# Performance work log

Measured on AMD Instinct MI355X. Metric: run time of the kernel, lower is better.

The kernel has to match this reference:

```python
import jax, jax.numpy as jnp
import numpy as np

LORA_SCALING = 2.0

def setup_inputs() -> dict:
    key = jax.random.key(0)
    ks = jax.random.split(key, 10)
    B, T, C, H, R, E = 4, 2048, 2048, 8192, 64, 4
    f32 = jnp.float32
    def w(k, shape, fan_in):
        return jax.random.normal(k, shape, f32) / np.float32(np.sqrt(fan_in))
    return {
        "x": jax.random.normal(ks[0], (B, T, C), f32),
        "x_prev": jax.random.normal(ks[1], (B, C), f32),
        "x_k": jax.random.uniform(ks[2], (1, 1, C), f32),
        "Router_ref": w(ks[3], (E - 1, C), C),
        "K_ref": w(ks[4], (C, H), C),          # right-multiplied: h @ K_ref
        "V_ref": w(ks[5], (H, C), H),          # right-multiplied: k @ V_ref
        "Ka": w(ks[6], (E, R, C), C),          # torch Linear layout [out,in]
        "Kb": w(ks[7], (E, H, R), R),
        "Va": w(ks[8], (E, R, H), H),
        "Vb": w(ks[9], (E, C, R), R),
        "MoETopk": 2,
        "MoECount": 4,
    }

def _moe_forward(x, x_prev, x_k, Router_ref, K_ref, V_ref, Ka, Kb, Va, Vb, MoETopk, MoECount):
    B, T, C = x.shape
    # token shift: mix each token with the previous one (x_prev seeds t=0)
    xx = jnp.concatenate([x_prev[:, None, :], x[:, :-1, :]], axis=1) - x
    h = (x + xx * x_k).reshape(-1, C)  # [N, C], N = B*T tokens
    N = h.shape[0]

    # router: expert 0 has implicit score 0, experts 1..E-1 come from Router_ref
    scores = h @ Router_ref.T                                   # [N, E-1]
    scores_all = jnp.concatenate([jnp.zeros((N, 1), h.dtype), scores], axis=-1)  # [N, E]
    if MoETopk < MoECount:
        topv, topi = jax.lax.top_k(scores_all, MoETopk)         # [N, K]
        gate = jax.nn.softmax(topv, axis=-1)
        gating_full = jnp.zeros_like(scores_all).at[
            jnp.arange(N)[:, None], topi].set(gate)             # [N, E], 0 for unselected
    else:
        gating_full = jax.nn.softmax(scores_all, axis=-1)

    # dense combine: gating weight is exactly 0 for unselected experts, so this
    # matches the original sparse dispatch + index_add math bit-for-bit in value.
    out = jnp.zeros_like(h)
    for e in range(MoECount):  # small fixed expert count
        k_e = jax.nn.relu(h @ K_ref + LORA_SCALING * (h @ Ka[e].T) @ Kb[e].T) ** 2  # [N, H]
        v_e = k_e @ V_ref + LORA_SCALING * (k_e @ Va[e].T) @ Vb[e].T                # [N, C]
        out = out + gating_full[:, e:e + 1] * v_e
    return out.reshape(B, T, C), x[:, -1, :]

def reference(x, x_prev, x_k, Router_ref, K_ref, V_ref, Ka, Kb, Va, Vb, MoETopk, MoECount):
    return _moe_forward(x, x_prev, x_k, Router_ref, K_ref, V_ref, Ka, Kb, Va, Vb,
                        int(MoETopk), int(MoECount))
```

## Files before the change

### kernel.cpp

```cpp
#include <hip/hip_runtime.h>


#define DEV_INLINE __device__ __forceinline__

typedef __attribute__((ext_vector_type(8))) short bf16x8;
typedef __attribute__((ext_vector_type(4))) float f32x4;

DEV_INLINE unsigned short f2bf(float f) {
  union { float f; unsigned int u; } v; v.f = f;
  unsigned int u = v.u;
  unsigned int r = (u + 0x7FFFu + ((u >> 16) & 1u)) >> 16;
  return (unsigned short)r;
}
DEV_INLINE float bf2f(unsigned short s) {
  union { unsigned int u; float f; } v; v.u = ((unsigned int)s) << 16;
  return v.f;
}


__global__ __launch_bounds__(256) void prep_kernel(
    const float* __restrict__ x, const float* __restrict__ x_prev,
    const float* __restrict__ x_k, unsigned short* __restrict__ h, int n0) {
  const int idx = blockIdx.x * 256 + threadIdx.x;
  const int c4 = idx & 511;
  const int gn = n0 + (idx >> 9);
  const int t  = gn & 2047;
  const int b  = gn >> 11;
  const float4 cur = ((const float4*)x)[(size_t)gn * 512 + c4];
  const float4 prv = (t == 0) ? ((const float4*)x_prev)[(b << 9) + c4]
                              : ((const float4*)x)[(size_t)gn * 512 - 512 + c4];
  const float4 k = ((const float4*)x_k)[c4];
  float hx = cur.x + (prv.x - cur.x) * k.x;
  float hy = cur.y + (prv.y - cur.y) * k.y;
  float hz = cur.z + (prv.z - cur.z) * k.z;
  float hw = cur.w + (prv.w - cur.w) * k.w;
  uint2 o;
  o.x = (unsigned int)f2bf(hx) | ((unsigned int)f2bf(hy) << 16);
  o.y = (unsigned int)f2bf(hz) | ((unsigned int)f2bf(hw) << 16);
  ((uint2*)h)[idx] = o;
}

__global__ __launch_bounds__(256) void xlast_kernel(
    const float* __restrict__ x, float* __restrict__ x_last) {
  const int i = blockIdx.x * 256 + threadIdx.x;
  const int b = i >> 9, c4 = i & 511;
  ((float4*)x_last)[i] =
      ((const float4*)x)[((size_t)b * 2048 + 2047) * 512 + c4];
}

__global__ __launch_bounds__(256) void transpose_cast(
    const float* __restrict__ in, unsigned short* __restrict__ outp,
    int rows, int cols) {
  __shared__ float tile[32][33];
  const int bx = blockIdx.x * 32, by = blockIdx.y * 32;
  const int tx = threadIdx.x, ty = threadIdx.y;
#pragma unroll
  for (int k = 0; k < 4; ++k)
    tile[ty + k * 8][tx] = in[(size_t)(by + ty + k * 8) * cols + bx + tx];
  __syncthreads();
#pragma unroll
  for (int k = 0; k < 4; ++k)
    outp[(size_t)(bx + ty + k * 8) * rows + by + tx] = f2bf(tile[tx][ty + k * 8]);
}

__global__ __launch_bounds__(256) void cast_bf16(
    const float* __restrict__ in, unsigned short* __restrict__ outp, int n4) {
  const int i = blockIdx.x * 256 + threadIdx.x;
  if (i >= n4) return;
  const float4 v = ((const float4*)in)[i];
  uint2 o;
  o.x = (unsigned int)f2bf(v.x) | ((unsigned int)f2bf(v.y) << 16);
  o.y = (unsigned int)f2bf(v.z) | ((unsigned int)f2bf(v.w) << 16);
  ((uint2*)outp)[i] = o;
}

__global__ void zero_page(unsigned int* zp) {
  if (threadIdx.x < 64) zp[threadIdx.x] = 0;
}

__global__ __launch_bounds__(256) void router_kernel(
    const float* __restrict__ x, const float* __restrict__ x_prev,
    const float* __restrict__ x_k, const float* __restrict__ Rt,
    int* __restrict__ tbl, int* __restrict__ etok,
    float* __restrict__ gate_tok, int MC, int n0) {
  const int lane = threadIdx.x & 63, wid = threadIdx.x >> 6;
  const int nl = blockIdx.x * 4 + wid;
  const int gn = n0 + nl;
  const int t = gn & 2047, b = gn >> 11;
  const float* cur = x + (size_t)gn * 2048;
  const float* prv = (t == 0) ? x_prev + (size_t)b * 2048 : cur - 2048;
  float hv[32];
#pragma unroll
  for (int j = 0; j < 32; ++j) {
    const int i = j * 64 + lane;
    const float xc = cur[i];
    hv[j] = xc + (prv[i] - xc) * x_k[i];
  }
  float s[4];
  s[0] = 0.f;
  for (int e = 1; e < 4; ++e) {
    const float* rrow = Rt + (size_t)(e - 1) * 2048;
    float a = 0.f;
#pragma unroll
    for (int j = 0; j < 32; ++j) a += hv[j] * rrow[j * 64 + lane];
#pragma unroll
    for (int d = 32; d >= 1; d >>= 1) a += __shfl_xor(a, d, 64);
    s[e] = a;
  }
  if (lane == 0) {
    int i1 = 0; float v1 = s[0];
    for (int e = 1; e < 4; ++e) if (s[e] > v1) { v1 = s[e]; i1 = e; }
    int i2 = -1; float v2 = -1e30f;
    for (int e = 0; e < 4; ++e) if (e != i1 && s[e] > v2) { v2 = s[e]; i2 = e; }
    const float ex = expf(v2 - v1);
    const float g1 = 1.f / (1.f + ex), g2 = ex / (1.f + ex);
    etok[nl] = i1;          etok[MC + nl] = i2;
    gate_tok[nl] = g1;      gate_tok[MC + nl] = g2;
    atomicAdd(&tbl[i1], 1); atomicAdd(&tbl[4 + i2], 1);
  }
}

__global__ void zero_hist(int* tbl) {
  if (threadIdx.x < 8) tbl[threadIdx.x] = 0;
}

__global__ __launch_bounds__(128) void seg_build(int* __restrict__ tbl, int MB) {
  const int tid = threadIdx.x;
  __shared__ int sbase[2][5];
  if (tid == 0) {
    for (int k = 0; k < 2; ++k) {
      int b = 0; sbase[k][0] = 0;
      for (int e = 0; e < 4; ++e) {
        b += ((tbl[k * 4 + e] + 127) >> 7) << 7;
        sbase[k][e + 1] = b;
      }
      for (int e = 0; e < 5; ++e) tbl[16 + k * 5 + e] = sbase[k][e];
    }
    for (int i = 0; i < 8; ++i) tbl[8 + i] = 0;
  }
  __syncthreads();
  int* bt = tbl + 32;
  for (int i = tid; i < 2 * MB; i += 128) {
    const int k = i / MB, row = (i % MB) * 128;
    int e = -1;
    for (int q = 0; q < 4; ++q)
      if (row >= sbase[k][q] && row < sbase[k][q + 1]) e = q;
    bt[i] = e;
  }
  int* tok = tbl + 32 + 2 * MB;
  for (int i = tid; i < 2 * MB * 128; i += 128) tok[i] = -1;
}

__global__ __launch_bounds__(256) void scatter_build(
    int* __restrict__ tbl, const int* __restrict__ etok, int MC, int MB) {
  const int t = blockIdx.x * 256 + threadIdx.x;
  if (t >= MC) return;
  int* tok = tbl + 32 + 2 * MB;
#pragma unroll
  for (int k = 0; k < 2; ++k) {
    const int e = etok[k * MC + t];
    const int r = atomicAdd(&tbl[8 + k * 4 + e], 1);
    tok[k * MB * 128 + tbl[16 + k * 5 + e] + r] = t;
  }
}

__global__ __launch_bounds__(512, 1) void gemm256(
    const unsigned short* __restrict__ A, int lda,
    const unsigned short* __restrict__ Bt, int ldb,
    unsigned short* __restrict__ C, int ldc, int K, int nbx) {
  __shared__ char smem[2][2][256 * 64 * 2];
  const int nwg = gridDim.x, wg = blockIdx.x;
  const int q = nwg >> 3, r = nwg & 7;
  const int xcd = wg & 7, loc = wg >> 3;
  const int swz = (xcd < r ? xcd * (q + 1) : r * (q + 1) + (xcd - r) * q) + loc;
  const int bx = swz % nbx, by = swz / nbx;
  const int m0 = by * 256, n0 = bx * 256;
  const int tid = threadIdx.x, lane = tid & 63;
  const int wid = tid >> 6, wr = wid >> 2, wc = wid & 3;

  int arow[4], scol[4];
#pragma unroll
  for (int i = 0; i < 4; ++i) {
    const int qq = i * 512 + tid;
    const int row = qq >> 3, w = qq & 7;
    arow[i] = row;
    scol[i] = (w ^ (row & 7)) * 8;
  }

  f32x4 acc[8][4] = {};

  auto stage = [&](int buf, int kt) {
#pragma unroll
    for (int i = 0; i < 4; ++i) {
      const unsigned short* src =
          A + (size_t)(m0 + arow[i]) * lda + kt + scol[i];
      __builtin_amdgcn_global_load_lds(
          (const __attribute__((address_space(1))) void*)src,
          (__attribute__((address_space(3))) void*)(
              &smem[buf][0][(i * 512 + tid) * 16]), 16, 0, 0);
    }
#pragma unroll
    for (int i = 0; i < 4; ++i) {
      const unsigned short* src =
          Bt + (size_t)(n0 + arow[i]) * ldb + kt + scol[i];
      __builtin_amdgcn_global_load_lds(
          (const __attribute__((address_space(1))) void*)src,
          (__attribute__((address_space(3))) void*)(
              &smem[buf][1][(i * 512 + tid) * 16]), 16, 0, 0);
    }
  };

  stage(0, 0);
  asm volatile("s_waitcnt vmcnt(0)" ::: "memory");
  __syncthreads();

  const int NT = K >> 6;
  for (int t = 0; t < NT; ++t) {
    const int cur = t & 1;
    if (t + 1 < NT) stage(cur ^ 1, (t + 1) << 6);
    const char* As = smem[cur][0];
    const char* Bs = smem[cur][1];
#pragma unroll
    for (int ks = 0; ks < 2; ++ks) {
#pragma unroll
      for (int mh = 0; mh < 2; ++mh) {
        bf16x8 af[4];
#pragma unroll
        for (int m = 0; m < 4; ++m) {
          const int row = wr * 128 + mh * 64 + m * 16 + (lane & 15);
          const int kb = (ks * 64 + ((lane >> 4) * 16)) ^ ((row & 7) << 4);
          af[m] = *(const bf16x8*)(As + row * 128 + kb);
        }
#pragma unroll
        for (int nh = 0; nh < 2; ++nh) {
          bf16x8 bf[2];
#pragma unroll
          for (int n = 0; n < 2; ++n) {
            const int row = wc * 64 + nh * 32 + n * 16 + (lane & 15);
            const int kb = (ks * 64 + ((lane >> 4) * 16)) ^ ((row & 7) << 4);
            bf[n] = *(const bf16x8*)(Bs + row * 128 + kb);
          }
          __builtin_amdgcn_s_setprio(1);
#pragma unroll
          for (int m = 0; m < 4; ++m)
#pragma unroll
            for (int n = 0; n < 2; ++n)
              acc[mh * 4 + m][nh * 2 + n] =
                  __builtin_amdgcn_mfma_f32_16x16x32_bf16(
                      af[m], bf[n], acc[mh * 4 + m][nh * 2 + n], 0, 0, 0);
          __builtin_amdgcn_s_setprio(0);
        }
      }
    }
    asm volatile("s_waitcnt vmcnt(0)" ::: "memory");
    __syncthreads();
  }

  const int cc = lane & 15, cr0 = (lane >> 4) * 4;
#pragma unroll
  for (int mf = 0; mf < 8; ++mf)
#pragma unroll
    for (int nf = 0; nf < 4; ++nf)
#pragma unroll
      for (int j = 0; j < 4; ++j) {
        const int grow = m0 + wr * 128 + mf * 16 + cr0 + j;
        const int gcol = n0 + wc * 64 + nf * 16 + cc;
        C[(size_t)grow * ldc + gcol] = f2bf(acc[mf][nf][j]);
      }
}

enum { EPI_BF16 = 0, EPI_KE = 1, EPI_GV = 2, EPI_VB0 = 3, EPI_VB1 = 4 };

template <int EPI>
__global__ __launch_bounds__(256) void gemm_bt(
    const unsigned short* __restrict__ A, int lda, long long strideAe,
    long long strideAslot,
    const unsigned short* __restrict__ B, int ldb, long long strideBe,
    const unsigned short* __restrict__ B2, const unsigned short* __restrict__ zp,
    void* __restrict__ Cp, int ldc, long long strideCslot,
    unsigned short* __restrict__ vatp, long long strideVat,
    const unsigned short* __restrict__ aux, int ldaux,
    const float* __restrict__ gate, const float* __restrict__ out2,
    float scale,
    const int* __restrict__ blocktab, const int* __restrict__ rowmap,
    const int* __restrict__ crowmap,
    int K, int nbx, int mbPerSlot, int PRr, int MCr) {
  constexpr int BM = 128, BN = 128, BK = 64;

  const int nwg = gridDim.x, wg = blockIdx.x;
  const int q = nwg >> 3, r = nwg & 7;
  const int xcd = wg & 7, loc = wg >> 3;
  const int swz = (xcd < r ? xcd * (q + 1) : r * (q + 1) + (xcd - r) * q) + loc;
  const int bx = swz % nbx;
  const int by = swz / nbx;

  int k = 0, byl = by;
  if (mbPerSlot > 0) { k = by / mbPerSlot; byl = by - k * mbPerSlot; }

  int e = 0;
  if (blocktab) { e = blocktab[by]; if (e < 0) return; }

  __shared__ alignas(16) char smem[(BM + BN) * BK * 2];
  char* As = smem;
  char* Bs = smem + BM * BK * 2;

  const unsigned short* Ae = A + (size_t)e * strideAe + (size_t)k * strideAslot;
  const bool vatBlk = (EPI == EPI_GV) && (B2 != nullptr) && (bx == nbx - 1);

  const int tid = threadIdx.x;
  const int lane = tid & 63;
  const int wid = tid >> 6;
  const int wr = wid >> 1, wc = wid & 1;
  const int m0 = byl * BM;
  const int bn0 = bx * BN;

  const int* tokA = rowmap ? rowmap + k * PRr : nullptr;
  int arow[4];
#pragma unroll
  for (int i = 0; i < 4; ++i) {
    const int row = (i * 256 + tid) >> 3;
    int rr = m0 + row;
    if (tokA) { rr = tokA[rr]; if (rr < 0) rr = 0; }
    arow[i] = rr;
  }

  f32x4 acc[4][4] = {};

  for (int kt = 0; kt < K; kt += BK) {
    __syncthreads();
#pragma unroll
    for (int i = 0; i < 4; ++i) {
      const int qq = i * 256 + tid;
      const int row = qq >> 3, w = qq & 7;
      const int g = w ^ (row & 7);
      const unsigned short* src = Ae + (size_t)arow[i] * lda + kt + g * 8;
      __builtin_amdgcn_global_load_lds(
          (const __attribute__((address_space(1))) void*)src,
          (__attribute__((address_space(3))) void*)(As + qq * 16), 16, 0, 0);
    }
#pragma unroll
    for (int i = 0; i < 4; ++i) {
      const int qq = i * 256 + tid;
      const int row = qq >> 3, w = qq & 7;
      const int g = w ^ (row & 7);
      const unsigned short* src;
      if (vatBlk) {
        src = (row < 64) ? B2 + ((size_t)e * 64 + row) * ldb + kt + g * 8
                         : (const unsigned short*)zp;
      } else {
        src = B + (size_t)e * strideBe + (size_t)(bn0 + row) * ldb + kt + g * 8;
      }
      __builtin_amdgcn_global_load_lds(
          (const __attribute__((address_space(1))) void*)src,
          (__attribute__((address_space(3))) void*)(Bs + qq * 16), 16, 0, 0);
    }
    asm volatile("s_waitcnt vmcnt(0)" ::: "memory");
    __syncthreads();

#pragma unroll
    for (int ks = 0; ks < 2; ++ks) {
      bf16x8 af[4], bfr[4];
#pragma unroll
      for (int m = 0; m < 4; ++m) {
        const int row = wr * 64 + m * 16 + (lane & 15);
        const int kb = (ks * 64 + ((lane >> 4) * 16)) ^ ((row & 7) << 4);
        af[m] = *(const bf16x8*)(As + row * 128 + kb);
      }
#pragma unroll
      for (int n = 0; n < 4; ++n) {
        const int row = wc * 64 + n * 16 + (lane & 15);
        const int kb = (ks * 64 + ((lane >> 4) * 16)) ^ ((row & 7) << 4);
        bfr[n] = *(const bf16x8*)(Bs + row * 128 + kb);
      }
#pragma unroll
      for (int m = 0; m < 4; ++m)
#pragma unroll
        for (int n = 0; n < 4; ++n)
          acc[m][n] = __builtin_amdgcn_mfma_f32_16x16x32_bf16(
              af[m], bfr[n], acc[m][n], 0, 0, 0);
    }
  }

  const int cc = lane & 15;
  const int cr0 = (lane >> 4) * 4;
#pragma unroll
  for (int m = 0; m < 4; ++m) {
#pragma unroll
    for (int n = 0; n < 4; ++n) {
#pragma unroll
      for (int j = 0; j < 4; ++j) {
        const int grow = m0 + wr * 64 + m * 16 + cr0 + j;
        const int lcol = wc * 64 + n * 16 + cc;
        const float v = acc[m][n][j];
        if constexpr (EPI == EPI_BF16) {
          ((unsigned short*)Cp)[(size_t)grow * ldc + bn0 + lcol] = f2bf(v);
        } else if constexpr (EPI == EPI_KE) {
          int ar = grow;
          if (tokA) { ar = tokA[grow]; if (ar < 0) ar = 0; }
          const float ksv = bf2f(aux[(size_t)ar * ldaux + bn0 + lcol]);
          float rr = ksv + 2.0f * v;
          rr = rr > 0.f ? rr : 0.f;
          ((unsigned short*)Cp + (size_t)k * strideCslot)
              [(size_t)grow * ldc + bn0 + lcol] = f2bf(rr * rr);
        } else if constexpr (EPI == EPI_GV) {
          if (vatBlk) {
            if (lcol < 64)
              (vatp + (size_t)k * strideVat)[(size_t)grow * 64 + lcol] = f2bf(v);
          } else {
            const int t = crowmap[k * PRr + grow];
            if (t >= 0) {
              const float g = gate[k * MCr + t] * scale;
              ((float*)Cp + (size_t)k * strideCslot)[(size_t)t * ldc + bn0 + lcol] =
                  g * v;
            }
          }
        } else if constexpr (EPI == EPI_VB0) {
          const int t = crowmap[grow];
          if (t >= 0) {
            const float g = gate[t] * scale;
            float* o = (float*)Cp + (size_t)t * ldc + bn0 + lcol;
            *o = *o + g * v;
          }
        } else {
          const int t = crowmap[grow];
          if (t >= 0) {
            const float g = gate[t] * scale;
            float* o = (float*)Cp + (size_t)t * ldc + bn0 + lcol;
            *o = *o + out2[(size_t)t * ldc + bn0 + lcol] + g * v;
          }
        }
      }
    }
  }
}

extern "C" void kernel_launch(void* const* d_in, const int* in_sizes, int n_in,
                              void* d_out, int out_size, void* d_ws,
                              size_t ws_size, hipStream_t stream) {
  (void)in_sizes; (void)n_in; (void)out_size;
  const float* x      = (const float*)d_in[0];
  const float* x_prev = (const float*)d_in[1];
  const float* x_k    = (const float*)d_in[2];
  const float* Router = (const float*)d_in[3];
  const float* K_ref  = (const float*)d_in[4];
  const float* V_ref  = (const float*)d_in[5];
  const float* Ka     = (const float*)d_in[6];
  const float* Kb     = (const float*)d_in[7];
  const float* Va     = (const float*)d_in[8];
  const float* Vb     = (const float*)d_in[9];

  static auto keep_bf16 = &gemm_bt<EPI_BF16>;
  (void)keep_bf16;

  constexpr int Bb = 4, T = 2048, C = 2048, H = 8192, R = 64, E = 4;
  constexpr int M = Bb * T;
  constexpr int NKL = H + E * R;

  const size_t PAD = 255;
  auto rnd = [&](size_t b) { return (b + PAD) & ~PAD; };
  const size_t persist = rnd((size_t)NKL * C * 2)
                       + rnd((size_t)C * H * 2)
                       + rnd((size_t)E * H * R * 2)
                       + rnd((size_t)E * R * H * 2)
                       + rnd((size_t)E * C * R * 2)
                       + rnd(256);

  int MC = 0;
  for (int cand = M; cand >= 1024; cand >>= 1) {
    const int mb = cand / 128 + 4;
    const long long pr = (long long)mb * 128;
    size_t keSpan = rnd((size_t)pr * H * 2);
    if (keSpan < rnd((size_t)cand * C * 2)) keSpan = rnd((size_t)cand * C * 2);
    size_t kslSpan = rnd((size_t)cand * NKL * 2);
    if (kslSpan < rnd((size_t)cand * C * 4)) kslSpan = rnd((size_t)cand * C * 4);
    const size_t need = persist + keSpan + kslSpan
                      + rnd((size_t)2 * pr * 64 * 2)
                      + rnd((size_t)(32 + 2 * mb + 2 * pr) * 4)
                      + rnd((size_t)2 * cand * 4)
                      + rnd((size_t)2 * cand * 4);
    if (need <= ws_size) { MC = cand; break; }
  }
  if (MC == 0) return;
  const int MB = MC / 128 + 4;
  const int PR = MB * 128;

  char* ws = (char*)d_ws;
  size_t off = 0;
  auto alloc = [&](size_t bytes) -> char* {
    char* p = ws + off; off += rnd(bytes); return p;
  };
  unsigned short* KtKa = (unsigned short*)alloc((size_t)NKL * C * 2);
  unsigned short* Vt   = (unsigned short*)alloc((size_t)C * H * 2);
  unsigned short* KbB  = (unsigned short*)alloc((size_t)E * H * R * 2);
  unsigned short* VaB  = (unsigned short*)alloc((size_t)E * R * H * 2);
  unsigned short* VbB  = (unsigned short*)alloc((size_t)E * C * R * 2);
  unsigned short* zp   = (unsigned short*)alloc(256);
  size_t keBytes = rnd((size_t)PR * H * 2);
  if (keBytes < rnd((size_t)MC * C * 2)) keBytes = rnd((size_t)MC * C * 2);
  unsigned short* k_e  = (unsigned short*)alloc(keBytes);
  size_t kslBytes = rnd((size_t)MC * NKL * 2);
  if (kslBytes < rnd((size_t)MC * C * 4)) kslBytes = rnd((size_t)MC * C * 4);
  unsigned short* ksl  = (unsigned short*)alloc(kslBytes);
  unsigned short* vat  = (unsigned short*)alloc((size_t)2 * PR * 64 * 2);
  int*            tbl  = (int*)alloc((size_t)(32 + 2 * MB + 2 * PR) * 4);
  int*            etok = (int*)alloc((size_t)2 * MC * 4);
  float*          gtok = (float*)alloc((size_t)2 * MC * 4);
  unsigned short* h_c  = k_e;
  float*          out2 = (float*)ksl;

  float* out    = (float*)d_out;
  float* x_last = out + (size_t)M * C;

  transpose_cast<<<dim3(H / 32, C / 32), dim3(32, 8), 0, stream>>>(K_ref, KtKa, C, H);
  cast_bf16<<<(E * R * C / 4 + 255) / 256, 256, 0, stream>>>(
      Ka, KtKa + (size_t)H * C, E * R * C / 4);
  transpose_cast<<<dim3(C / 32, H / 32), dim3(32, 8), 0, stream>>>(V_ref, Vt, H, C);
  cast_bf16<<<(E * H * R / 4 + 255) / 256, 256, 0, stream>>>(Kb, KbB, E * H * R / 4);
  cast_bf16<<<(E * R * H / 4 + 255) / 256, 256, 0, stream>>>(Va, VaB, E * R * H / 4);
  cast_bf16<<<(E * C * R / 4 + 255) / 256, 256, 0, stream>>>(Vb, VbB, E * C * R / 4);
  zero_page<<<1, 64, 0, stream>>>((unsigned int*)zp);
  xlast_kernel<<<Bb * C / 4 / 256, 256, 0, stream>>>(x, x_last);

  for (int c0 = 0; c0 < M; c0 += MC) {
    float* outc = out + (size_t)c0 * C;
    prep_kernel<<<MC * C / 4 / 256, 256, 0, stream>>>(x, x_prev, x_k, h_c, c0);
    zero_hist<<<1, 64, 0, stream>>>(tbl);
    router_kernel<<<MC / 4, 256, 0, stream>>>(x, x_prev, x_k, Router, tbl,
                                              etok, gtok, MC, c0);
    seg_build<<<1, 128, 0, stream>>>(tbl, MB);
    scatter_build<<<(MC + 255) / 256, 256, 0, stream>>>(tbl, etok, MC, MB);

    const int* bt  = tbl + 32;
    const int* tok = tbl + 32 + 2 * MB;

    gemm256<<<(MC / 256) * (NKL / 256), 512, 0, stream>>>(
        h_c, C, KtKa, C, ksl, NKL, C, NKL / 256);

    for (int k = 0; k < 2; ++k) {
      const int* btk  = bt + k * MB;
      const int* tokk = tok + k * PR;
      const float* gk = gtok + (size_t)k * MC;

      gemm_bt<EPI_KE><<<(H / 128) * MB, 256, 0, stream>>>(
          ksl + H, NKL, 64, 0, KbB, R, (long long)H * R, nullptr, nullptr,
          k_e, H, 0, nullptr, 0, ksl, NKL, nullptr, nullptr, 0.f,
          btk, tokk, nullptr, R, H / 128, 0, PR, MC);

      gemm_bt<EPI_GV><<<(C / 128 + 1) * MB, 256, 0, stream>>>(
          k_e, H, 0, 0, Vt, H, 0, VaB, zp,
          (k == 0) ? (void*)outc : (void*)out2, C, 0,
          vat + (size_t)k * PR * 64, 0, nullptr, 0, gk, nullptr, 1.0f,
          btk, nullptr, tokk, H, C / 128 + 1, 0, PR, MC);

      if (k == 0) {
        gemm_bt<EPI_VB0><<<(C / 128) * MB, 256, 0, stream>>>(
            vat, 64, 0, 0, VbB, R, (long long)C * R, nullptr, nullptr,
            outc, C, 0, nullptr, 0, nullptr, 0, gk, nullptr, 2.0f,
            btk, nullptr, tokk, R, C / 128, 0, PR, MC);
      } else {
        gemm_bt<EPI_VB1><<<(C / 128) * MB, 256, 0, stream>>>(
            vat + (size_t)PR * 64, 64, 0, 0, VbB, R, (long long)C * R,
            nullptr, nullptr, outc, C, 0, nullptr, 0, nullptr, 0,
            gk, out2, 2.0f,
            btk, nullptr, tokk, R, C / 128, 0, PR, MC);
      }
    }
  }
}
```

Measured before the change: 2.029 ms.

## Add ping-pong pipelined 256x256 GEMM with quarter-staged LDS loads for K projection

Introduces gemm8p, a 256x256-tile bf16 GEMM that splits each 64-wide K step into four quarter phases. Each phase issues direct global-to-LDS loads for the next tiles while running MFMAs on the current quadrant, with barriers between phases and wave priority raised around the MFMAs. It replaces gemm256 for the h @ [K_ref|Ka] projection, aiming to hide memory latency behind compute. The trade is more barriers per K step and fragile waitcnt bookkeeping.

```diff
diff --git a/kernel.cpp b/kernel.cpp
--- a/kernel.cpp
+++ b/kernel.cpp
@@ -162,6 +162,128 @@
     const int r = atomicAdd(&tbl[8 + k * 4 + e], 1);
     tok[k * MB * 128 + tbl[16 + k * 5 + e] + r] = t;
   }
+}
+
+__global__ __launch_bounds__(512, 1) void gemm8p(
+    const unsigned short* __restrict__ A, int lda,
+    const unsigned short* __restrict__ Bt, int ldb,
+    unsigned short* __restrict__ C, int ldc, int K, int nbx) {
+  __shared__ alignas(16) char As_[2][32768];
+  __shared__ alignas(16) char Bs_[2][32768];
+  const int nwg = gridDim.x, wg = blockIdx.x;
+  const int q = nwg >> 3, r = nwg & 7;
+  const int xcd = wg & 7, loc = wg >> 3;
+  const int swz = (xcd < r ? xcd * (q + 1) : r * (q + 1) + (xcd - r) * q) + loc;
+  const int bx = swz % nbx, by = swz / nbx;
+  const int m0 = by * 256, n0 = bx * 256;
+  const int tid = threadIdx.x, lane = tid & 63;
+  const int wid = tid >> 6, wr = wid >> 2, wc = wid & 3;
+
+  auto stageA = [&](int buf, int kt, int rbase) {
+#pragma unroll
+    for (int j = 0; j < 2; ++j) {
+      const int idx = j * 512 + tid;
+      const int s = idx >> 3, w = idx & 7;
+      const int g = s >> 6, lrow = rbase + (s & 63);
+      const unsigned short* src =
+          A + (size_t)(m0 + g * 128 + lrow) * lda + kt + ((w ^ (lrow & 7)) * 8);
+      __builtin_amdgcn_global_load_lds(
+          (const __attribute__((address_space(1))) void*)src,
+          (__attribute__((address_space(3))) void*)(
+              &As_[buf][g * 16384 + lrow * 128 + w * 16]), 16, 0, 0);
+    }
+  };
+  auto stageB = [&](int buf, int kt, int nq) {
+#pragma unroll
+    for (int j = 0; j < 2; ++j) {
+      const int idx = j * 512 + tid;
+      const int s = idx >> 3, w = idx & 7;
+      const int g = s >> 5, half = g >> 1, grp = g & 1;
+      const int lrow = grp * 64 + nq * 32 + (s & 31);
+      const unsigned short* src =
+          Bt + (size_t)(n0 + half * 128 + lrow) * ldb + kt +
+          ((w ^ (lrow & 7)) * 8);
+      __builtin_amdgcn_global_load_lds(
+          (const __attribute__((address_space(1))) void*)src,
+          (__attribute__((address_space(3))) void*)(
+              &Bs_[buf][half * 16384 + lrow * 128 + w * 16]), 16, 0, 0);
+    }
+  };
+
+  f32x4 acc[8][4] = {};
+  bf16x8 afr[4][2], bfr[2][2];
+
+#define READ_A(buf, mq)                                                      \
+  _Pragma("unroll") for (int mf = 0; mf < 4; ++mf)                           \
+  _Pragma("unroll") for (int ks = 0; ks < 2; ++ks) {                         \
+    const int lr = (mq) * 64 + mf * 16 + (lane & 15);                        \
+    afr[mf][ks] = *(const bf16x8*)(&As_[buf][wr * 16384 + lr * 128 +         \
+        ((ks * 64 + ((lane >> 4) * 16)) ^ ((lr & 7) << 4))]);                \
+  }
+#define READ_B(buf, nq)                                                      \
+  _Pragma("unroll") for (int nf = 0; nf < 2; ++nf)                           \
+  _Pragma("unroll") for (int ks = 0; ks < 2; ++ks) {                         \
+    const int gcl = wc * 64 + (nq) * 32 + nf * 16 + (lane & 15);             \
+    const int hf = gcl >> 7, lr = gcl & 127;                                 \
+    bfr[nf][ks] = *(const bf16x8*)(&Bs_[buf][hf * 16384 + lr * 128 +         \
+        ((ks * 64 + ((lane >> 4) * 16)) ^ ((lr & 7) << 4))]);                \
+  }
+#define DO_MFMA(mq, nq)                                                      \
+  __builtin_amdgcn_s_setprio(1);                                             \
+  _Pragma("unroll") for (int ks = 0; ks < 2; ++ks)                           \
+  _Pragma("unroll") for (int mf = 0; mf < 4; ++mf)                           \
+  _Pragma("unroll") for (int nf = 0; nf < 2; ++nf)                           \
+    acc[(mq) * 4 + mf][(nq) * 2 + nf] =                                      \
+        __builtin_amdgcn_mfma_f32_16x16x32_bf16(                             \
+            afr[mf][ks], bfr[nf][ks], acc[(mq) * 4 + mf][(nq) * 2 + nf],     \
+            0, 0, 0);                                                        \
+  __builtin_amdgcn_s_setprio(0);
+#define GBAR asm volatile("s_barrier" ::: "memory")
+
+  const int NT = K >> 6;
+  stageA(0, 0, 0); stageA(0, 0, 64); stageB(0, 0, 0); stageB(0, 0, 1);
+  stageA(1, 64, 0); stageB(1, 64, 1);
+  asm volatile("s_waitcnt vmcnt(4)" ::: "memory");
+  GBAR;
+
+  for (int t = 0; t < NT; ++t) {
+    const int buf = t & 1, o = buf ^ 1;
+    const int kt1 = (t + 1) << 6, kt2 = (t + 2) << 6;
+    READ_A(buf, 0); READ_B(buf, 0);
+    if (t + 1 < NT) stageA(o, kt1, 64);
+    DO_MFMA(0, 0);
+    GBAR;
+    READ_B(buf, 1);
+    if (t + 1 < NT) stageB(o, kt1, 0);
+    DO_MFMA(0, 1);
+    GBAR;
+    READ_A(buf, 1);
+    if (t + 2 < NT) stageA(buf, kt2, 0);
+    DO_MFMA(1, 1);
+    GBAR;
+    READ_B(buf, 0);
+    if (t + 2 < NT) stageB(buf, kt2, 1);
+    DO_MFMA(1, 0);
+    if (t + 2 < NT) { asm volatile("s_waitcnt vmcnt(4)" ::: "memory"); }
+    else            { asm volatile("s_waitcnt vmcnt(0)" ::: "memory"); }
+    GBAR;
+  }
+#undef READ_A
+#undef READ_B
+#undef DO_MFMA
+#undef GBAR
+
+  const int cc = lane & 15, cr0 = (lane >> 4) * 4;
+#pragma unroll
+  for (int mf = 0; mf < 8; ++mf)
+#pragma unroll
+    for (int nf = 0; nf < 4; ++nf)
+#pragma unroll
+      for (int j = 0; j < 4; ++j) {
+        const int grow = m0 + wr * 128 + mf * 16 + cr0 + j;
+        const int gcol = n0 + wc * 64 + nf * 16 + cc;
+        C[(size_t)grow * ldc + gcol] = f2bf(acc[mf][nf][j]);
+      }
 }
 
 __global__ __launch_bounds__(512, 1) void gemm256(
@@ -533,7 +655,7 @@
     const int* bt  = tbl + 32;
     const int* tok = tbl + 32 + 2 * MB;
 
-    gemm256<<<(MC / 256) * (NKL / 256), 512, 0, stream>>>(
+    gemm8p<<<(MC / 256) * (NKL / 256), 512, 0, stream>>>(
         h_c, C, KtKa, C, ksl, NKL, C, NKL / 256);
 
     for (int k = 0; k < 2; ++k) {
```

New measurement: 2.026 ms. About the same (-0.1%).
